# Kernel optimization log

Hardware: AMD Instinct MI355X
Metric: run time of the kernel (lower is better)

Reference implementation:

```python
import jax, jax.numpy as jnp
import numpy as np

EPS = 1e-5
NUM_HEADS = 8

def _inorm(x):
    # InstanceNorm1d (affine=False): normalize over last (length) axis per (B, C)
    m = x.mean(axis=-1, keepdims=True)
    v = x.var(axis=-1, keepdims=True)  # biased variance, as torch instance norm
    return (x - m) * jax.lax.rsqrt(v + EPS)

def setup_inputs() -> dict:
    key = jax.random.key(0)
    ks = jax.random.split(key, 12)
    B, Nl, HW = 4, 1024, 4096
    Cl, Cv, Ck, Cval, Cout = 512, 512, 256, 256, 256
    w = lambda k, shape: (jax.random.normal(k, shape, jnp.float32) * 0.02)
    return {
        "l": jax.random.normal(ks[0], (B, Nl, Cl), jnp.float32),
        "x": jax.random.normal(ks[1], (B, HW, Cv), jnp.float32),
        "Wq": w(ks[2], (Ck, Cl)),   "bq": w(ks[3], (Ck,)),
        "Wk": w(ks[4], (Ck, Cv)),   "bk": w(ks[5], (Ck,)),
        "Wv": w(ks[6], (Cval, Cv)), "bv": w(ks[7], (Cval,)),
        "Ww": w(ks[8], (Cout, Cval)), "bw": w(ks[9], (Cout,)),
    }

def reference(l, x, Wq, bq, Wk, bk, Wv, bv, Ww, bw):
    H = NUM_HEADS
    Ck = Wq.shape[0]
    Cv = Wv.shape[0]
    dk, dv = Ck // H, Cv // H
    B, Nl, _ = l.shape
    HW = x.shape[1]

    # 1x1 Conv1d == per-position linear
    q = jnp.einsum('blc,kc->blk', l, Wq) + bq                     # [B, Nl, Ck]
    k = jnp.einsum('bnc,kc->bkn', x, Wk) + bk[None, :, None]      # [B, Ck, HW]
    k = _inorm(k)                                                  # InstanceNorm over HW
    v = jnp.einsum('bnc,kc->bkn', x, Wv) + bv[None, :, None]      # [B, Cv, HW]

    q = q.reshape(B, Nl, H, dk).transpose(0, 2, 1, 3)             # [B, H, Nl, dk]
    k = k.reshape(B, H, dk, HW)                                   # [B, H, dk, HW]
    v = v.reshape(B, H, dv, HW)                                   # [B, H, dv, HW]

    sim = jnp.einsum('bhld,bhdn->bhln', q, k) * (Ck ** -0.5)      # [B, H, Nl, HW]
    att = jax.nn.softmax(sim, axis=-1)
    out = jnp.einsum('bhln,bhdn->bhld', att, v)                   # [B, H, Nl, dv]

    out = out.transpose(0, 2, 1, 3).reshape(B, Nl, Cv)            # [B, Nl, Cv]
    out = jnp.einsum('blc,oc->bol', out, Ww) + bw[None, :, None]  # [B, Cout, Nl]
    out = _inorm(out)                                              # InstanceNorm over Nl
    return out.transpose(0, 2, 1)                                  # [B, Nl, Cout]
```

## Files before the change

### kernel.cpp

```cpp
#include <hip/hip_runtime.h>

constexpr int Bn = 4, NL = 1024, HWn = 4096, NH = 8;

typedef __attribute__((ext_vector_type(8))) short bf16x8;
typedef __attribute__((ext_vector_type(4))) float f32x4;
#define MFMA16 __builtin_amdgcn_mfma_f32_16x16x32_bf16

__device__ __forceinline__ float b2f(unsigned short u) {
  union { unsigned int i; float f; } x; x.i = ((unsigned int)u) << 16; return x.f;
}
__device__ __forceinline__ unsigned short f2b(float f) {
  union { float f; unsigned int i; } x; x.f = f;
  unsigned int r = x.i + 0x7fffu + ((x.i >> 16) & 1u);
  return (unsigned short)(r >> 16);
}
__device__ __forceinline__ unsigned short f2b_rtz(float f) {
  union { float f; unsigned int i; } x; x.f = f;
  return (unsigned short)(x.i >> 16);
}
__device__ __forceinline__ void load4f(const float* p, float* o) {
  float4 v = *(const float4*)p; o[0] = v.x; o[1] = v.y; o[2] = v.z; o[3] = v.w;
}

__global__ __launch_bounds__(256) void conv_bf16(const float* __restrict__ src,
    unsigned short* __restrict__ dst, int n)
{
  int i = (blockIdx.x * 256 + threadIdx.x) * 4;
  if (i < n) {
    float4 v = *(const float4*)(src + i);
    ushort4 o; o.x = f2b(v.x); o.y = f2b(v.y); o.z = f2b(v.z); o.w = f2b(v.w);
    *(ushort4*)(dst + i) = o;
  }
}

__global__ __launch_bounds__(256) void conv_w3(const float* __restrict__ Wk,
    const float* __restrict__ Wv, const float* __restrict__ Wq,
    unsigned short* __restrict__ wkb, unsigned short* __restrict__ wvb,
    unsigned short* __restrict__ wqb)
{
  const float* src = blockIdx.y == 0 ? Wk : (blockIdx.y == 1 ? Wv : Wq);
  unsigned short* dst = blockIdx.y == 0 ? wkb : (blockIdx.y == 1 ? wvb : wqb);
  int i = (blockIdx.x * 256 + threadIdx.x) * 4;
  float4 v = *(const float4*)(src + i);
  ushort4 o; o.x = f2b(v.x); o.y = f2b(v.y); o.z = f2b(v.z); o.w = f2b(v.w);
  *(ushort4*)(dst + i) = o;
}

__global__ __launch_bounds__(256, 2) void gemm128(
    const unsigned short* __restrict__ xbf, const unsigned short* __restrict__ lbf,
    const unsigned short* __restrict__ wkb, const unsigned short* __restrict__ wvb,
    const unsigned short* __restrict__ wqb,
    const float* __restrict__ bk, const float* __restrict__ bv, const float* __restrict__ bq,
    unsigned short* __restrict__ khb, unsigned short* __restrict__ vhb,
    unsigned short* __restrict__ qbuf)
{
  __shared__ unsigned short As[128 * 32];
  __shared__ unsigned short Bs[128 * 32];
  const int id = blockIdx.x;
  const int mode = id < 256 ? 0 : (id < 512 ? 1 : 2);
  const int local = id - (mode == 0 ? 0 : (mode == 1 ? 256 : 512));
  const int rb = local >> 1, cb = local & 1;
  const int m0 = rb * 128, n0 = cb * 128;
  const unsigned short* A = (mode == 2) ? lbf : xbf;
  const unsigned short* W = (mode == 0) ? wkb : (mode == 1 ? wvb : wqb);
  const float* bias = (mode == 0) ? bk : (mode == 1 ? bv : bq);

  const int tid = threadIdx.x, w = tid >> 6, lane = tid & 63;
  const int quad = lane >> 4, l15 = lane & 15;
  const int wr = w >> 1, wc = w & 1;

  const int p0 = tid, p1 = tid + 256;
  const int am0 = p0 >> 2, ak0 = (p0 & 3) * 8;
  const int am1 = p1 >> 2, ak1 = (p1 & 3) * 8;

  f32x4 acc[4][4];
#pragma unroll
  for (int i = 0; i < 4; ++i)
#pragma unroll
    for (int j = 0; j < 4; ++j) acc[i][j] = (f32x4){0.f, 0.f, 0.f, 0.f};

  bf16x8 ar0 = *(const bf16x8*)(A + (size_t)(m0 + am0) * 512 + ak0);
  bf16x8 ar1 = *(const bf16x8*)(A + (size_t)(m0 + am1) * 512 + ak1);
  bf16x8 br0 = *(const bf16x8*)(W + (size_t)(n0 + am0) * 512 + ak0);
  bf16x8 br1 = *(const bf16x8*)(W + (size_t)(n0 + am1) * 512 + ak1);

  for (int kt = 0; kt < 16; ++kt) {
    __syncthreads();
    *(bf16x8*)&As[p0 * 8] = ar0;
    *(bf16x8*)&As[p1 * 8] = ar1;
    *(bf16x8*)&Bs[p0 * 8] = br0;
    *(bf16x8*)&Bs[p1 * 8] = br1;
    if (kt < 15) {
      int k0 = (kt + 1) * 32;
      ar0 = *(const bf16x8*)(A + (size_t)(m0 + am0) * 512 + k0 + ak0);
      ar1 = *(const bf16x8*)(A + (size_t)(m0 + am1) * 512 + k0 + ak1);
      br0 = *(const bf16x8*)(W + (size_t)(n0 + am0) * 512 + k0 + ak0);
      br1 = *(const bf16x8*)(W + (size_t)(n0 + am1) * 512 + k0 + ak1);
    }
    __syncthreads();
    bf16x8 af[4], bf[4];
#pragma unroll
    for (int fr = 0; fr < 4; ++fr)
      af[fr] = *(const bf16x8*)&As[(wr * 64 + fr * 16 + l15) * 32 + quad * 8];
#pragma unroll
    for (int fc = 0; fc < 4; ++fc)
      bf[fc] = *(const bf16x8*)&Bs[(wc * 64 + fc * 16 + l15) * 32 + quad * 8];
#pragma unroll
    for (int fr = 0; fr < 4; ++fr)
#pragma unroll
      for (int fc = 0; fc < 4; ++fc)
        acc[fr][fc] = MFMA16(af[fr], bf[fc], acc[fr][fc], 0, 0, 0);
  }

  float bb[4];
#pragma unroll
  for (int fc = 0; fc < 4; ++fc) bb[fc] = bias[n0 + wc * 64 + fc * 16 + l15];
  unsigned short* dst = (mode == 0) ? khb : (mode == 1 ? vhb : qbuf);
#pragma unroll
  for (int fr = 0; fr < 4; ++fr) {
#pragma unroll
    for (int fc = 0; fc < 4; ++fc) {
      int col = n0 + wc * 64 + fc * 16 + l15;
#pragma unroll
      for (int r = 0; r < 4; ++r) {
        int row = m0 + wr * 64 + fr * 16 + quad * 4 + r;
        unsigned short val = f2b(acc[fr][fc][r] + bb[fc]);
        if (mode == 2) {
          dst[(size_t)row * 256 + col] = val;
        } else {
          int b = row >> 12, n = row & 4095, h = col >> 5, d = col & 31;
          dst[((size_t)(b * 8 + h) * 4096 + n) * 32 + d] = val;
        }
      }
    }
  }
}

__global__ __launch_bounds__(256) void kvstats(const unsigned short* __restrict__ khb,
    const unsigned short* __restrict__ vhb,
    float* __restrict__ ksum, float* __restrict__ kss, float* __restrict__ vcs)
{
  const int which = blockIdx.x >> 5, bh = blockIdx.x & 31, seg = blockIdx.y;
  const int t = threadIdx.x, d = t & 31, g = t >> 5;
  __shared__ float rs[256], rss[256];
  if (which == 0) {
    const unsigned short* base = khb + (size_t)bh * 131072 + (size_t)seg * 512 * 32;
    float s = 0.f, ss = 0.f;
    for (int i = 0; i < 64; ++i) {
      float v = b2f(base[(size_t)(g + i * 8) * 32 + d]);
      s += v; ss += v * v;
    }
    rs[t] = s; rss[t] = ss;
    __syncthreads();
    if (t < 32) {
      float a = 0.f, b = 0.f;
      for (int g2 = 0; g2 < 8; ++g2) { a += rs[t + g2 * 32]; b += rss[t + g2 * 32]; }
      atomicAdd(&ksum[bh * 32 + t], a);
      atomicAdd(&kss[bh * 32 + t], b);
    }
  } else {
    const unsigned short* base = vhb + (size_t)bh * 131072 + (size_t)seg * 512 * 32;
    float s = 0.f;
    for (int i = 0; i < 64; ++i) s += b2f(base[(size_t)(g + i * 8) * 32 + d]);
    rs[t] = s;
    __syncthreads();
    if (t < 32) {
      float a = 0.f;
      for (int g2 = 0; g2 < 8; ++g2) a += rs[t + g2 * 32];
      vcs[seg * 1024 + bh * 32 + t] = a;
    }
  }
}

__global__ __launch_bounds__(256) void kfinal(const float* __restrict__ ksum,
    const float* __restrict__ kss, float* __restrict__ krstd)
{
  int i = blockIdx.x * 256 + threadIdx.x;
  float m = ksum[i] * (1.f / 4096.f);
  float var = kss[i] * (1.f / 4096.f) - m * m;
  krstd[i] = rsqrtf(var + 1e-5f);
}

__global__ __launch_bounds__(256) void vpack(const unsigned short* __restrict__ vh,
    unsigned short* __restrict__ vfrag)
{
  __shared__ unsigned short vt[256][42];
  const int bh = blockIdx.x >> 4, slab = blockIdx.x & 15;
  const unsigned short* src = vh + ((size_t)bh * 4096 + slab * 256) * 32;
  const int t = threadIdx.x;
#pragma unroll
  for (int i = 0; i < 4; ++i) {
    int p = i * 256 + t;
    int n = p >> 2, piece = p & 3;
    uint4 v = *(const uint4*)(src + (size_t)n * 32 + piece * 8);
    unsigned int* lrow = (unsigned int*)&vt[n][piece * 8];
    lrow[0] = v.x; lrow[1] = v.y; lrow[2] = v.z; lrow[3] = v.w;
  }
  __syncthreads();
#pragma unroll
  for (int i = 0; i < 4; ++i) {
    int op = i * 256 + t;
    int lanep = op & 63, rest = op >> 6;
    int dvt = rest & 1, kh2 = (rest >> 1) & 1, chunkl = rest >> 2;
    int lq = lanep >> 4, ll = lanep & 15;
    unsigned short o[8];
#pragma unroll
    for (int j = 0; j < 8; ++j)
      o[j] = vt[chunkl * 64 + kh2 * 32 + lq * 8 + j][dvt * 16 + ll];
    size_t dst = ((((size_t)bh * 64 + slab * 4 + chunkl) * 2 + kh2) * 2 + dvt) * 512 + lanep * 8;
    *(bf16x8*)(vfrag + dst) = *(const bf16x8*)o;
  }
}

__global__ __launch_bounds__(256, 3) void attn2(const unsigned short* __restrict__ qbuf,
    const unsigned short* __restrict__ khb, const unsigned short* __restrict__ vfrag,
    const float* __restrict__ krstd, const float* __restrict__ vcs,
    float* __restrict__ po, float* __restrict__ pd)
{
  const int bh = blockIdx.x, b = bh >> 3, h = bh & 7;
  const int lsuper = blockIdx.y, half = blockIdx.z;
  const int tid = threadIdx.x, w = tid >> 6, lane = tid & 63;
  const int quad = lane >> 4, l15 = lane & 15;

  __shared__ unsigned short kb_s[2048];
  __shared__ unsigned short vb_s[2048];
  __shared__ unsigned short ps[4][64][72];

  bf16x8 qa[4];
  {
    float fold[8];
    const float* rp = krstd + bh * 32 + quad * 8;
#pragma unroll
    for (int j = 0; j < 8; ++j) fold[j] = rp[j] * 0.0625f;
#pragma unroll
    for (int lf = 0; lf < 4; ++lf) {
      int l = lsuper * 256 + w * 64 + lf * 16 + l15;
      bf16x8 qr = *(const bf16x8*)(qbuf + ((size_t)(b * NL + l)) * 256 + h * 32 + quad * 8);
      const unsigned short* qq = (const unsigned short*)&qr;
      unsigned short tmp[8];
#pragma unroll
      for (int j = 0; j < 8; ++j) tmp[j] = f2b(b2f(qq[j]) * fold[j]);
      qa[lf] = *(const bf16x8*)tmp;
    }
  }

  float drow[4][4];
  f32x4 acc[4][2];
#pragma unroll
  for (int lf = 0; lf < 4; ++lf) {
#pragma unroll
    for (int r = 0; r < 4; ++r) drow[lf][r] = 0.f;
    acc[lf][0] = (f32x4){0.f,0.f,0.f,0.f};
    acc[lf][1] = (f32x4){0.f,0.f,0.f,0.f};
  }

  const unsigned short* kcbase = khb + (size_t)bh * 131072 + (size_t)half * 512 * 32;
  const unsigned short* vcbase = vfrag + (size_t)bh * 131072 + (size_t)half * 8 * 2048;

  bf16x8 kreg = *(const bf16x8*)(kcbase + tid * 8);
  bf16x8 vreg = *(const bf16x8*)(vcbase + tid * 8);

  for (int c = 0; c < 8; ++c) {
    __syncthreads();
    *(bf16x8*)&kb_s[tid * 8] = kreg;
    *(bf16x8*)&vb_s[tid * 8] = vreg;
    if (c < 7) {
      kreg = *(const bf16x8*)(kcbase + (c + 1) * 2048 + tid * 8);
      vreg = *(const bf16x8*)(vcbase + (c + 1) * 2048 + tid * 8);
    }
    __syncthreads();

    bf16x8 kb[4];
#pragma unroll
    for (int t = 0; t < 4; ++t)
      kb[t] = *(const bf16x8*)&kb_s[(t * 16 + l15) * 32 + quad * 8];
    bf16x8 vb[4];
#pragma unroll
    for (int i = 0; i < 4; ++i)
      vb[i] = *(const bf16x8*)&vb_s[i * 512 + lane * 8];

    f32x4 z = (f32x4){0.f,0.f,0.f,0.f};
#pragma unroll
    for (int lf = 0; lf < 4; ++lf) {
      f32x4 sv[4];
#pragma unroll
      for (int t = 0; t < 4; ++t) sv[t] = MFMA16(qa[lf], kb[t], z, 0, 0, 0);
#pragma unroll
      for (int r = 0; r < 4; ++r) {
        float e0 = __expf(sv[0][r]), e1 = __expf(sv[1][r]);
        float e2 = __expf(sv[2][r]), e3 = __expf(sv[3][r]);
        drow[lf][r] += (e0 + e1) + (e2 + e3);
        int row = lf * 16 + quad * 4 + r;
        ps[w][row][l15]      = f2b_rtz(e0 - 1.0f);
        ps[w][row][16 + l15] = f2b_rtz(e1 - 1.0f);
        ps[w][row][32 + l15] = f2b_rtz(e2 - 1.0f);
        ps[w][row][48 + l15] = f2b_rtz(e3 - 1.0f);
      }
    }
    asm volatile("s_waitcnt lgkmcnt(0)" ::: "memory");
#pragma unroll
    for (int lf = 0; lf < 4; ++lf) {
#pragma unroll
      for (int kh2 = 0; kh2 < 2; ++kh2) {
        bf16x8 pa = *(const bf16x8*)&ps[w][lf * 16 + l15][kh2 * 32 + quad * 8];
#pragma unroll
        for (int dvt = 0; dvt < 2; ++dvt)
          acc[lf][dvt] = MFMA16(pa, vb[kh2 * 2 + dvt], acc[lf][dvt], 0, 0, 0);
      }
    }
  }

  const float* vc = vcs + half * 1024 + bh * 32;
  float cs0 = vc[l15], cs1 = vc[16 + l15];
#pragma unroll
  for (int lf = 0; lf < 4; ++lf)
#pragma unroll
    for (int r = 0; r < 4; ++r) {
      acc[lf][0][r] += cs0;
      acc[lf][1][r] += cs1;
    }

  const size_t PDo = (size_t)half * 32768 + (size_t)bh * 1024;
#pragma unroll
  for (int lf = 0; lf < 4; ++lf) {
#pragma unroll
    for (int r = 0; r < 4; ++r) {
      float sv = drow[lf][r];
      sv += __shfl_xor(sv, 1, 16);
      sv += __shfl_xor(sv, 2, 16);
      sv += __shfl_xor(sv, 4, 16);
      sv += __shfl_xor(sv, 8, 16);
      int l = lsuper * 256 + w * 64 + lf * 16 + quad * 4 + r;
      size_t base = (PDo + l) * 32;
      po[base + l15]      = acc[lf][0][r];
      po[base + 16 + l15] = acc[lf][1][r];
      if (l15 == 0) pd[PDo + l] = sv;
    }
  }
}

__global__ __launch_bounds__(256) void combine8(const float* __restrict__ po,
    const float* __restrict__ pd, float* __restrict__ ao)
{
  int gid = blockIdx.x * 256 + threadIdx.x;
  int dv = gid & 31, l = (gid >> 5) & (NL - 1), h = (gid >> 15) & 7, b = gid >> 18;
  size_t r = ((size_t)(b * 8 + h)) * 1024 + l;
  float d = 0.f, o = 0.f;
#pragma unroll
  for (int half = 0; half < 8; ++half) {
    size_t rr = (size_t)half * 32768 + r;
    d += pd[rr];
    o += po[rr * 32 + dv];
  }
  ao[((size_t)(b * NL) + l) * 256 + h * 32 + dv] = o / d;
}

__global__ __launch_bounds__(256) void gemm_nt(const float* __restrict__ A, int lda,
    const float* __restrict__ W, int ldw, const float* __restrict__ bias,
    float* __restrict__ C, int ldc, int K)
{
  __shared__ float As[32][68];
  __shared__ float Ws[32][68];
  const int bm = blockIdx.x * 64, bn = blockIdx.y * 64;
  const int tid = threadIdx.x;
  const int ty = tid >> 4, tx = tid & 15;
  float acc[4][4] = {};
  for (int k0 = 0; k0 < K; k0 += 32) {
#pragma unroll
    for (int it = 0; it < 2; ++it) {
      int c = tid + it * 256;
      int m = c >> 3, kq = (c & 7) << 2;
      float av[4], wv[4];
      load4f(A + (size_t)(bm + m) * lda + k0 + kq, av);
      load4f(W + (size_t)(bn + m) * ldw + k0 + kq, wv);
      As[kq + 0][m] = av[0]; As[kq + 1][m] = av[1]; As[kq + 2][m] = av[2]; As[kq + 3][m] = av[3];
      Ws[kq + 0][m] = wv[0]; Ws[kq + 1][m] = wv[1]; Ws[kq + 2][m] = wv[2]; Ws[kq + 3][m] = wv[3];
    }
    __syncthreads();
#pragma unroll
    for (int kk = 0; kk < 32; ++kk) {
      float a[4], w[4];
      *(float4*)a = *(const float4*)&As[kk][ty << 2];
      *(float4*)w = *(const float4*)&Ws[kk][tx << 2];
#pragma unroll
      for (int i = 0; i < 4; ++i)
#pragma unroll
        for (int j = 0; j < 4; ++j)
          acc[i][j] = fmaf(a[i], w[j], acc[i][j]);
    }
    __syncthreads();
  }
  const int row0 = bm + (ty << 2), col0 = bn + (tx << 2);
  float bb[4];
#pragma unroll
  for (int j = 0; j < 4; ++j) bb[j] = bias[col0 + j];
#pragma unroll
  for (int i = 0; i < 4; ++i) {
    float4 o;
    o.x = acc[i][0] + bb[0]; o.y = acc[i][1] + bb[1];
    o.z = acc[i][2] + bb[2]; o.w = acc[i][3] + bb[3];
    *(float4*)(C + (size_t)(row0 + i) * ldc + col0) = o;
  }
}

__global__ __launch_bounds__(256) void stats_kernel(const float* __restrict__ X,
    long batchStride, int rowsPerBlock,
    float* __restrict__ sum, float* __restrict__ sumsq)
{
  const int b = blockIdx.x, c = threadIdx.x;
  const long r0 = (long)blockIdx.y * rowsPerBlock;
  const float* base = X + (long)b * batchStride + r0 * 256 + c;
  float s = 0.f, ss = 0.f;
  for (int r = 0; r < rowsPerBlock; ++r) {
    float v = base[(long)r * 256];
    s += v; ss += v * v;
  }
  atomicAdd(&sum[b * 256 + c], s);
  atomicAdd(&sumsq[b * 256 + c], ss);
}

__global__ __launch_bounds__(256) void finalize_stats(const float* __restrict__ sum,
    const float* __restrict__ sumsq, float invR,
    float* __restrict__ mean, float* __restrict__ rstd)
{
  int i = blockIdx.x * 256 + threadIdx.x;
  float m = sum[i] * invR;
  float v = sumsq[i] * invR - m * m;
  mean[i] = m;
  rstd[i] = rsqrtf(v + 1e-5f);
}

__global__ __launch_bounds__(256) void final_out(const float* __restrict__ proj,
    const float* __restrict__ mean, const float* __restrict__ rstd,
    float* __restrict__ out)
{
  const int b = blockIdx.x, o = threadIdx.x;
  const int l1 = blockIdx.y * 16;
  const float m = mean[b * 256 + o], r = rstd[b * 256 + o];
  for (int i = 0; i < 16; ++i) {
    size_t idx = ((size_t)(b * NL + l1 + i)) * 256 + o;
    out[idx] = (proj[idx] - m) * r;
  }
}

extern "C" void kernel_launch(void* const* d_in, const int* in_sizes, int n_in,
                              void* d_out, int out_size, void* d_ws, size_t ws_size,
                              hipStream_t stream)
{
  const float* l  = (const float*)d_in[0];
  const float* x  = (const float*)d_in[1];
  const float* Wq = (const float*)d_in[2];
  const float* bq = (const float*)d_in[3];
  const float* Wk = (const float*)d_in[4];
  const float* bk = (const float*)d_in[5];
  const float* Wv = (const float*)d_in[6];
  const float* bv = (const float*)d_in[7];
  const float* Ww = (const float*)d_in[8];
  const float* bw = (const float*)d_in[9];
  float* out = (float*)d_out;

  unsigned short* up = (unsigned short*)d_ws;
  unsigned short* xbf   = up;
  unsigned short* lbf   = xbf   + 8388608;
  unsigned short* wkb   = lbf   + 2097152;
  unsigned short* wvb   = wkb   + 131072;
  unsigned short* wqb   = wvb   + 131072;
  unsigned short* qbuf  = wqb   + 131072;
  unsigned short* khb   = qbuf  + 1048576;
  unsigned short* vhb   = khb   + 4194304;
  unsigned short* vfrag = vhb   + 4194304;
  float* F     = (float*)((char*)d_ws + 49020928);
  float* krstd = F;
  float* vcs   = krstd + 1024;
  float* po    = vcs + 8192;
  float* pd    = po + 8388608;
  float* ao    = pd + 262144;
  float* pj    = ao + 1048576;
  float* st    = pj + 1048576;
  float* ksum  = st;          float* kss   = st + 1024;
  float* psum  = st + 2048;   float* psq   = st + 3072;
  float* pmean = st + 4096;   float* prstd = st + 5120;

  hipMemsetAsync(st, 0, 4096 * sizeof(float), stream);

  dim3 blk(256);
  conv_bf16<<<8192, blk, 0, stream>>>(x,  xbf, 8388608);
  conv_bf16<<<2048, blk, 0, stream>>>(l,  lbf, 2097152);
  conv_w3<<<dim3(128, 3), blk, 0, stream>>>(Wk, Wv, Wq, wkb, wvb, wqb);
  gemm128<<<576, blk, 0, stream>>>(xbf, lbf, wkb, wvb, wqb, bk, bv, bq, khb, vhb, qbuf);
  kvstats<<<dim3(64, 8), blk, 0, stream>>>(khb, vhb, ksum, kss, vcs);
  kfinal<<<4, blk, 0, stream>>>(ksum, kss, krstd);
  vpack<<<512, blk, 0, stream>>>(vhb, vfrag);
  attn2<<<dim3(32, 4, 8), blk, 0, stream>>>(qbuf, khb, vfrag, krstd, vcs, po, pd);
  combine8<<<4096, blk, 0, stream>>>(po, pd, ao);
  gemm_nt<<<dim3(64, 4), blk, 0, stream>>>(ao, 256, Ww, 256, bw, pj, 256, 256);
  stats_kernel<<<dim3(4, 64), blk, 0, stream>>>(pj, (long)NL * 256, 16, psum, psq);
  finalize_stats<<<4, blk, 0, stream>>>(psum, psq, 1.0f / NL, pmean, prstd);
  final_out<<<dim3(4, 64), blk, 0, stream>>>(pj, pmean, prstd, out);
}
```

Baseline: 209.6 us.

## Use split-bf16 MFMA output projection, exp2 softmax, smaller P tile for occupancy

Replaces the fp32 SIMT output-projection GEMM with an MFMA kernel that splits activations and Ww into bf16 hi/lo parts and sums three cross products to keep near-fp32 accuracy. The attention kernel folds log2(e) into the Q scaling and uses native exp2. It also shrinks the per-wave P staging buffer to a single 16-row slice so occupancy can rise from 3 to 4 blocks per CU. The trade-off is extra LDS waits inside the inner loop and extra hi/lo buffers and conversions.

```diff
diff --git a/kernel.cpp b/kernel.cpp
--- a/kernel.cpp
+++ b/kernel.cpp
@@ -5,6 +5,8 @@
 typedef __attribute__((ext_vector_type(8))) short bf16x8;
 typedef __attribute__((ext_vector_type(4))) float f32x4;
 #define MFMA16 __builtin_amdgcn_mfma_f32_16x16x32_bf16
+
+extern "C" __device__ float __ocml_native_exp2_f32(float);
 
 __device__ __forceinline__ float b2f(unsigned short u) {
   union { unsigned int i; float f; } x; x.i = ((unsigned int)u) << 16; return x.f;
@@ -17,9 +19,6 @@
 __device__ __forceinline__ unsigned short f2b_rtz(float f) {
   union { float f; unsigned int i; } x; x.f = f;
   return (unsigned short)(x.i >> 16);
-}
-__device__ __forceinline__ void load4f(const float* p, float* o) {
-  float4 v = *(const float4*)p; o[0] = v.x; o[1] = v.y; o[2] = v.z; o[3] = v.w;
 }
 
 __global__ __launch_bounds__(256) void conv_bf16(const float* __restrict__ src,
@@ -33,14 +32,28 @@
   }
 }
 
-__global__ __launch_bounds__(256) void conv_w3(const float* __restrict__ Wk,
+__global__ __launch_bounds__(256) void conv_w4(const float* __restrict__ Wk,
     const float* __restrict__ Wv, const float* __restrict__ Wq,
+    const float* __restrict__ Ww,
     unsigned short* __restrict__ wkb, unsigned short* __restrict__ wvb,
-    unsigned short* __restrict__ wqb)
-{
+    unsigned short* __restrict__ wqb,
+    unsigned short* __restrict__ wwh, unsigned short* __restrict__ wwl)
+{
+  int i = (blockIdx.x * 256 + threadIdx.x) * 4;
+  if (blockIdx.y == 3) {
+    if (i >= 65536) return;
+    float4 v = *(const float4*)(Ww + i);
+    ushort4 hi, lo;
+    hi.x = f2b(v.x); lo.x = f2b(v.x - b2f(hi.x));
+    hi.y = f2b(v.y); lo.y = f2b(v.y - b2f(hi.y));
+    hi.z = f2b(v.z); lo.z = f2b(v.z - b2f(hi.z));
+    hi.w = f2b(v.w); lo.w = f2b(v.w - b2f(hi.w));
+    *(ushort4*)(wwh + i) = hi;
+    *(ushort4*)(wwl + i) = lo;
+    return;
+  }
   const float* src = blockIdx.y == 0 ? Wk : (blockIdx.y == 1 ? Wv : Wq);
   unsigned short* dst = blockIdx.y == 0 ? wkb : (blockIdx.y == 1 ? wvb : wqb);
-  int i = (blockIdx.x * 256 + threadIdx.x) * 4;
   float4 v = *(const float4*)(src + i);
   ushort4 o; o.x = f2b(v.x); o.y = f2b(v.y); o.z = f2b(v.z); o.w = f2b(v.w);
   *(ushort4*)(dst + i) = o;
@@ -212,7 +225,7 @@
   }
 }
 
-__global__ __launch_bounds__(256, 3) void attn2(const unsigned short* __restrict__ qbuf,
+__global__ __launch_bounds__(256, 4) void attn3(const unsigned short* __restrict__ qbuf,
     const unsigned short* __restrict__ khb, const unsigned short* __restrict__ vfrag,
     const float* __restrict__ krstd, const float* __restrict__ vcs,
     float* __restrict__ po, float* __restrict__ pd)
@@ -224,14 +237,14 @@
 
   __shared__ unsigned short kb_s[2048];
   __shared__ unsigned short vb_s[2048];
-  __shared__ unsigned short ps[4][64][72];
+  __shared__ unsigned short ps[4][16][72];
 
   bf16x8 qa[4];
   {
     float fold[8];
     const float* rp = krstd + bh * 32 + quad * 8;
 #pragma unroll
-    for (int j = 0; j < 8; ++j) fold[j] = rp[j] * 0.0625f;
+    for (int j = 0; j < 8; ++j) fold[j] = rp[j] * (0.0625f * 1.44269504f);
 #pragma unroll
     for (int lf = 0; lf < 4; ++lf) {
       int l = lsuper * 256 + w * 64 + lf * 16 + l15;
@@ -287,26 +300,26 @@
       for (int t = 0; t < 4; ++t) sv[t] = MFMA16(qa[lf], kb[t], z, 0, 0, 0);
 #pragma unroll
       for (int r = 0; r < 4; ++r) {
-        float e0 = __expf(sv[0][r]), e1 = __expf(sv[1][r]);
-        float e2 = __expf(sv[2][r]), e3 = __expf(sv[3][r]);
+        float e0 = __ocml_native_exp2_f32(sv[0][r]);
+        float e1 = __ocml_native_exp2_f32(sv[1][r]);
+        float e2 = __ocml_native_exp2_f32(sv[2][r]);
+        float e3 = __ocml_native_exp2_f32(sv[3][r]);
         drow[lf][r] += (e0 + e1) + (e2 + e3);
-        int row = lf * 16 + quad * 4 + r;
+        int row = quad * 4 + r;
         ps[w][row][l15]      = f2b_rtz(e0 - 1.0f);
         ps[w][row][16 + l15] = f2b_rtz(e1 - 1.0f);
         ps[w][row][32 + l15] = f2b_rtz(e2 - 1.0f);
         ps[w][row][48 + l15] = f2b_rtz(e3 - 1.0f);
       }
-    }
-    asm volatile("s_waitcnt lgkmcnt(0)" ::: "memory");
-#pragma unroll
-    for (int lf = 0; lf < 4; ++lf) {
+      asm volatile("s_waitcnt lgkmcnt(0)" ::: "memory");
 #pragma unroll
       for (int kh2 = 0; kh2 < 2; ++kh2) {
-        bf16x8 pa = *(const bf16x8*)&ps[w][lf * 16 + l15][kh2 * 32 + quad * 8];
+        bf16x8 pa = *(const bf16x8*)&ps[w][l15][kh2 * 32 + quad * 8];
 #pragma unroll
         for (int dvt = 0; dvt < 2; ++dvt)
           acc[lf][dvt] = MFMA16(pa, vb[kh2 * 2 + dvt], acc[lf][dvt], 0, 0, 0);
       }
+      asm volatile("s_waitcnt lgkmcnt(0)" ::: "memory");
     }
   }
 
@@ -340,7 +353,8 @@
 }
 
 __global__ __launch_bounds__(256) void combine8(const float* __restrict__ po,
-    const float* __restrict__ pd, float* __restrict__ ao)
+    const float* __restrict__ pd, unsigned short* __restrict__ aoh,
+    unsigned short* __restrict__ aol)
 {
   int gid = blockIdx.x * 256 + threadIdx.x;
   int dv = gid & 31, l = (gid >> 5) & (NL - 1), h = (gid >> 15) & 7, b = gid >> 18;
@@ -352,55 +366,73 @@
     d += pd[rr];
     o += po[rr * 32 + dv];
   }
-  ao[((size_t)(b * NL) + l) * 256 + h * 32 + dv] = o / d;
-}
-
-__global__ __launch_bounds__(256) void gemm_nt(const float* __restrict__ A, int lda,
-    const float* __restrict__ W, int ldw, const float* __restrict__ bias,
-    float* __restrict__ C, int ldc, int K)
-{
-  __shared__ float As[32][68];
-  __shared__ float Ws[32][68];
-  const int bm = blockIdx.x * 64, bn = blockIdx.y * 64;
-  const int tid = threadIdx.x;
-  const int ty = tid >> 4, tx = tid & 15;
-  float acc[4][4] = {};
-  for (int k0 = 0; k0 < K; k0 += 32) {
-#pragma unroll
-    for (int it = 0; it < 2; ++it) {
-      int c = tid + it * 256;
-      int m = c >> 3, kq = (c & 7) << 2;
-      float av[4], wv[4];
-      load4f(A + (size_t)(bm + m) * lda + k0 + kq, av);
-      load4f(W + (size_t)(bn + m) * ldw + k0 + kq, wv);
-      As[kq + 0][m] = av[0]; As[kq + 1][m] = av[1]; As[kq + 2][m] = av[2]; As[kq + 3][m] = av[3];
-      Ws[kq + 0][m] = wv[0]; Ws[kq + 1][m] = wv[1]; Ws[kq + 2][m] = wv[2]; Ws[kq + 3][m] = wv[3];
-    }
-    __syncthreads();
-#pragma unroll
-    for (int kk = 0; kk < 32; ++kk) {
-      float a[4], w[4];
-      *(float4*)a = *(const float4*)&As[kk][ty << 2];
-      *(float4*)w = *(const float4*)&Ws[kk][tx << 2];
-#pragma unroll
-      for (int i = 0; i < 4; ++i)
-#pragma unroll
-        for (int j = 0; j < 4; ++j)
-          acc[i][j] = fmaf(a[i], w[j], acc[i][j]);
-    }
-    __syncthreads();
-  }
-  const int row0 = bm + (ty << 2), col0 = bn + (tx << 2);
-  float bb[4];
-#pragma unroll
-  for (int j = 0; j < 4; ++j) bb[j] = bias[col0 + j];
-#pragma unroll
-  for (int i = 0; i < 4; ++i) {
-    float4 o;
-    o.x = acc[i][0] + bb[0]; o.y = acc[i][1] + bb[1];
-    o.z = acc[i][2] + bb[2]; o.w = acc[i][3] + bb[3];
-    *(float4*)(C + (size_t)(row0 + i) * ldc + col0) = o;
-  }
+  o = o / d;
+  unsigned short hi = f2b(o);
+  size_t idx = ((size_t)(b * NL) + l) * 256 + h * 32 + dv;
+  aoh[idx] = hi;
+  aol[idx] = f2b(o - b2f(hi));
+}
+
+__global__ __launch_bounds__(256) void gemm_proj(
+    const unsigned short* __restrict__ aoh, const unsigned short* __restrict__ aol,
+    const unsigned short* __restrict__ wwh, const unsigned short* __restrict__ wwl,
+    const float* __restrict__ bw, float* __restrict__ pj)
+{
+  __shared__ unsigned short As[64 * 32];
+  __shared__ unsigned short Bs[128 * 32];
+  const int bm = blockIdx.x * 64, bn = blockIdx.y * 128;
+  const int tid = threadIdx.x, w = tid >> 6, lane = tid & 63;
+  const int quad = lane >> 4, l15 = lane & 15;
+  const int wr = w >> 1, wc = w & 1;
+  const int arow = tid >> 2, apiece = (tid & 3) * 8;
+
+  f32x4 acc[2][4];
+#pragma unroll
+  for (int i = 0; i < 2; ++i)
+#pragma unroll
+    for (int j = 0; j < 4; ++j) acc[i][j] = (f32x4){0.f, 0.f, 0.f, 0.f};
+
+  for (int pair = 0; pair < 3; ++pair) {
+    const unsigned short* A = (pair == 1) ? aol : aoh;
+    const unsigned short* Bm = (pair == 2) ? wwl : wwh;
+    for (int kt = 0; kt < 8; ++kt) {
+      int k0 = kt * 32;
+      __syncthreads();
+      *(bf16x8*)&As[tid * 8] = *(const bf16x8*)(A + (size_t)(bm + arow) * 256 + k0 + apiece);
+#pragma unroll
+      for (int it = 0; it < 2; ++it) {
+        int p = tid + it * 256;
+        int brow = p >> 2, bpiece = (p & 3) * 8;
+        *(bf16x8*)&Bs[p * 8] = *(const bf16x8*)(Bm + (size_t)(bn + brow) * 256 + k0 + bpiece);
+      }
+      __syncthreads();
+      bf16x8 af[2], bf[4];
+#pragma unroll
+      for (int fr = 0; fr < 2; ++fr)
+        af[fr] = *(const bf16x8*)&As[(wr * 32 + fr * 16 + l15) * 32 + quad * 8];
+#pragma unroll
+      for (int fc = 0; fc < 4; ++fc)
+        bf[fc] = *(const bf16x8*)&Bs[(wc * 64 + fc * 16 + l15) * 32 + quad * 8];
+#pragma unroll
+      for (int fr = 0; fr < 2; ++fr)
+#pragma unroll
+        for (int fc = 0; fc < 4; ++fc)
+          acc[fr][fc] = MFMA16(af[fr], bf[fc], acc[fr][fc], 0, 0, 0);
+    }
+  }
+
+#pragma unroll
+  for (int fr = 0; fr < 2; ++fr)
+#pragma unroll
+    for (int fc = 0; fc < 4; ++fc) {
+      int col = bn + wc * 64 + fc * 16 + l15;
+      float bb = bw[col];
+#pragma unroll
+      for (int r = 0; r < 4; ++r) {
+        int row = bm + wr * 32 + fr * 16 + quad * 4 + r;
+        pj[(size_t)row * 256 + col] = acc[fr][fc][r] + bb;
+      }
+    }
 }
 
 __global__ __launch_bounds__(256) void stats_kernel(const float* __restrict__ X,
@@ -469,13 +501,16 @@
   unsigned short* khb   = qbuf  + 1048576;
   unsigned short* vhb   = khb   + 4194304;
   unsigned short* vfrag = vhb   + 4194304;
-  float* F     = (float*)((char*)d_ws + 49020928);
+  unsigned short* aoh   = vfrag + 4194304;
+  unsigned short* aol   = aoh   + 1048576;
+  unsigned short* wwh   = aol   + 1048576;
+  unsigned short* wwl   = wwh   + 65536;
+  float* F     = (float*)((char*)d_ws + 53477376);
   float* krstd = F;
   float* vcs   = krstd + 1024;
   float* po    = vcs + 8192;
   float* pd    = po + 8388608;
-  float* ao    = pd + 262144;
-  float* pj    = ao + 1048576;
+  float* pj    = pd + 262144;
   float* st    = pj + 1048576;
   float* ksum  = st;          float* kss   = st + 1024;
   float* psum  = st + 2048;   float* psq   = st + 3072;
@@ -486,14 +521,14 @@
   dim3 blk(256);
   conv_bf16<<<8192, blk, 0, stream>>>(x,  xbf, 8388608);
   conv_bf16<<<2048, blk, 0, stream>>>(l,  lbf, 2097152);
-  conv_w3<<<dim3(128, 3), blk, 0, stream>>>(Wk, Wv, Wq, wkb, wvb, wqb);
+  conv_w4<<<dim3(128, 4), blk, 0, stream>>>(Wk, Wv, Wq, Ww, wkb, wvb, wqb, wwh, wwl);
   gemm128<<<576, blk, 0, stream>>>(xbf, lbf, wkb, wvb, wqb, bk, bv, bq, khb, vhb, qbuf);
   kvstats<<<dim3(64, 8), blk, 0, stream>>>(khb, vhb, ksum, kss, vcs);
   kfinal<<<4, blk, 0, stream>>>(ksum, kss, krstd);
   vpack<<<512, blk, 0, stream>>>(vhb, vfrag);
-  attn2<<<dim3(32, 4, 8), blk, 0, stream>>>(qbuf, khb, vfrag, krstd, vcs, po, pd);
-  combine8<<<4096, blk, 0, stream>>>(po, pd, ao);
-  gemm_nt<<<dim3(64, 4), blk, 0, stream>>>(ao, 256, Ww, 256, bw, pj, 256, 256);
+  attn3<<<dim3(32, 4, 8), blk, 0, stream>>>(qbuf, khb, vfrag, krstd, vcs, po, pd);
+  combine8<<<4096, blk, 0, stream>>>(po, pd, aoh, aol);
+  gemm_proj<<<dim3(64, 2), blk, 0, stream>>>(aoh, aol, wwh, wwl, bw, pj);
   stats_kernel<<<dim3(4, 64), blk, 0, stream>>>(pj, (long)NL * 256, 16, psum, psq);
   finalize_stats<<<4, blk, 0, stream>>>(psum, psq, 1.0f / NL, pmean, prstd);
   final_out<<<dim3(4, 64), blk, 0, stream>>>(pj, pmean, prstd, out);
```

New measurement: 223.9 us. 6.8% more time.
